# Kernel tuning notes

Measured on AMD Instinct MI355X. Metric: run time of the kernel, lower is better.

The kernel has to match this reference:

```python
import jax, jax.numpy as jnp
import numpy as np

T, B = 128, 256
E, H, C = 128, 1024, 10
VOCAB = 10


def setup_inputs() -> dict:
    key = jax.random.key(0)
    ks = jax.random.split(key, 12)
    x = jax.random.randint(ks[0], (T, B), 0, VOCAB)
    emb = jax.random.normal(ks[1], (VOCAB, E), dtype=jnp.float32)
    Wgx = jax.random.normal(ks[2], (E, H), dtype=jnp.float32) / np.sqrt(E)
    Wgh = jax.random.normal(ks[3], (H, H), dtype=jnp.float32) / np.sqrt(H)
    Wix = jax.random.normal(ks[4], (E, H), dtype=jnp.float32) / np.sqrt(E)
    Wih = jax.random.normal(ks[5], (H, H), dtype=jnp.float32) / np.sqrt(H)
    Wfx = jax.random.normal(ks[6], (E, H), dtype=jnp.float32) / np.sqrt(E)
    Wfh = jax.random.normal(ks[7], (H, H), dtype=jnp.float32) / np.sqrt(H)
    Wox = jax.random.normal(ks[8], (E, H), dtype=jnp.float32) / np.sqrt(E)
    Woh = jax.random.normal(ks[9], (H, H), dtype=jnp.float32) / np.sqrt(H)
    Wph = jax.random.normal(ks[10], (H, C), dtype=jnp.float32) / np.sqrt(H)
    bg = jnp.zeros((H,), jnp.float32)
    bi = jnp.zeros((H,), jnp.float32)
    bf = jnp.zeros((H,), jnp.float32)
    bo = jnp.zeros((H,), jnp.float32)
    bp = jnp.zeros((C,), jnp.float32)
    return dict(x=x, emb=emb, Wgx=Wgx, Wgh=Wgh, Wix=Wix, Wih=Wih, Wfx=Wfx,
                Wfh=Wfh, Wox=Wox, Woh=Woh, bg=bg, bi=bi, bf=bf, bo=bo,
                Wph=Wph, bp=bp)


def reference(x, emb, Wgx, Wgh, Wix, Wih, Wfx, Wfh, Wox, Woh,
              bg, bi, bf, bo, Wph, bp):
    Bsz = x.shape[1]
    Hn = Wgh.shape[0]
    # Fuse the 8 gate matmuls into 2 GEMMs per step (same math, concat order g,i,f,o)
    Wx = jnp.concatenate([Wgx, Wix, Wfx, Wox], axis=1)  # [E, 4H]
    Wh = jnp.concatenate([Wgh, Wih, Wfh, Woh], axis=1)  # [H, 4H]
    b = jnp.concatenate([bg, bi, bf, bo], axis=0)        # [4H]

    def step(carry, xt):
        state, hidden = carry
        e = emb[xt]                                      # [B, E]
        pre = e @ Wx + hidden @ Wh + b                   # [B, 4H]
        g = jnp.tanh(pre[:, :Hn])
        i = jax.nn.sigmoid(pre[:, Hn:2 * Hn])
        f = jax.nn.sigmoid(pre[:, 2 * Hn:3 * Hn])
        o = jax.nn.sigmoid(pre[:, 3 * Hn:])
        state = g * i + state * f
        hidden = jnp.tanh(state) * o
        return (state, hidden), None

    init = (jnp.zeros((Bsz, Hn), jnp.float32), jnp.zeros((Bsz, Hn), jnp.float32))
    (state, hidden), _ = jax.lax.scan(step, init, x)
    # Original detaches hidden/state before the output projection
    hidden = jax.lax.stop_gradient(hidden)
    return hidden @ Wph + bp                             # [B, C]
```

## Files before the change

kernel.cpp:

```cpp
#include <hip/hip_runtime.h>

typedef __bf16 bf16;
typedef __bf16 bf16x8 __attribute__((ext_vector_type(8)));
typedef float  f32x4  __attribute__((ext_vector_type(4)));

#define T_STEPS 128
#define BATCH   256
#define HD      1024
#define N4H     4096
#define EMB_D   128

__device__ __forceinline__ float fast_sigmoid(float x) {
    return 1.0f / (1.0f + __expf(-x));
}
__device__ __forceinline__ float fast_tanh(float x) {
    return 1.0f - 2.0f / (__expf(2.0f * x) + 1.0f);
}

__global__ void build_P(const float* __restrict__ emb,
                        const float* __restrict__ Wgx, const float* __restrict__ Wix,
                        const float* __restrict__ Wfx, const float* __restrict__ Wox,
                        const float* __restrict__ bg,  const float* __restrict__ bi,
                        const float* __restrict__ bfv, const float* __restrict__ bo,
                        float* __restrict__ P)
{
    int n = blockIdx.x * 256 + threadIdx.x;
    int v  = n >> 12;
    int nn = n & (N4H - 1);
    int hcol = nn >> 2, gate = nn & 3;
    const float* Wx = (gate == 0) ? Wgx : (gate == 1) ? Wix : (gate == 2) ? Wfx : Wox;
    const float* bb = (gate == 0) ? bg  : (gate == 1) ? bi  : (gate == 2) ? bfv : bo;
    float s = bb[hcol];
    for (int e = 0; e < EMB_D; ++e)
        s += emb[v * EMB_D + e] * Wx[e * HD + hcol];
    P[n] = s;
}

__global__ void build_W(const float* __restrict__ Wgh, const float* __restrict__ Wih,
                        const float* __restrict__ Wfh, const float* __restrict__ Woh,
                        bf16* __restrict__ WhpT)
{
    __shared__ float tile[64][65];
    int bid  = blockIdx.x;
    int gate = bid >> 8;
    int t2   = bid & 255;
    int kt = t2 >> 4, ht = t2 & 15;
    const float* W = (gate == 0) ? Wgh : (gate == 1) ? Wih : (gate == 2) ? Wfh : Woh;
    int tid = threadIdx.x;
    #pragma unroll
    for (int it = 0; it < 16; ++it) {
        int idx = it * 256 + tid;
        int kk = idx >> 6, hh = idx & 63;
        tile[kk][hh] = W[(size_t)(kt * 64 + kk) * HD + ht * 64 + hh];
    }
    __syncthreads();
    #pragma unroll
    for (int it = 0; it < 16; ++it) {
        int idx = it * 256 + tid;
        int hh = idx >> 6, kk = idx & 63;
        int n = (ht * 64 + hh) * 4 + gate;
        WhpT[(size_t)n * HD + kt * 64 + kk] = (bf16)tile[kk][hh];
    }
}

__global__ __launch_bounds__(512, 2)
void lstm_main(const int* __restrict__ x, const float* __restrict__ P,
               const bf16* __restrict__ WhpT, bf16* __restrict__ hbuf,
               int* __restrict__ ctl)
{
    __shared__ bf16  Blds[32][1024];
    __shared__ float red[4][64][20];

    const int tid  = threadIdx.x;
    const int lane = tid & 63;
    const int wid  = tid >> 6;
    const int w    = wid & 3;
    const int kh   = wid >> 2;
    const int frow = lane & 15;
    const int kgrp = lane >> 4;
    const int bid  = blockIdx.x;
    const int g    = bid >> 5;
    const int j    = bid & 31;

    int* bar = ctl + g * 16;

    const bf16* Abase = WhpT + (size_t)(j * 128 + w * 32 + frow) * HD + kh * 512 + kgrp * 8;
    bf16x8 Ar[2][16];
    #pragma unroll
    for (int fn = 0; fn < 2; ++fn)
        #pragma unroll
        for (int ks = 0; ks < 16; ++ks)
            Ar[fn][ks] = *(const bf16x8*)(Abase + fn * 16 * HD + ks * 32);

    const int pn0  = j * 128 + w * 32 + kgrp * 4;
    const int hc0  = j * 32 + w * 8 + kgrp;
    const int mr0  = g * 32 + frow;
    const int xorf = frow & 7;
    char* BB = (char*)&Blds[0][0];

    float st[2][2] = {{0.f, 0.f}, {0.f, 0.f}};

    for (int t = 0; t < T_STEPS; ++t) {
        f32x4 acc[2][2];
        if (kh == 0) {
            int xv0 = x[t * BATCH + mr0];
            int xv1 = x[t * BATCH + mr0 + 16];
            acc[0][0] = *(const f32x4*)(P + (size_t)xv0 * N4H + pn0);
            acc[0][1] = *(const f32x4*)(P + (size_t)xv1 * N4H + pn0);
            acc[1][0] = *(const f32x4*)(P + (size_t)xv0 * N4H + pn0 + 16);
            acc[1][1] = *(const f32x4*)(P + (size_t)xv1 * N4H + pn0 + 16);
        } else {
            f32x4 z = {0.f, 0.f, 0.f, 0.f};
            acc[0][0] = z; acc[0][1] = z; acc[1][0] = z; acc[1][1] = z;
        }

        if (t > 0) {
            if (tid == 0) {
                const int tgt = 32 * t;
                long guard = 0;
                while (__hip_atomic_load(bar, __ATOMIC_RELAXED, __HIP_MEMORY_SCOPE_AGENT) < tgt
                       && ++guard < (1L << 24)) {}
            }
            __syncthreads();
            const char* src = (const char*)(hbuf + (size_t)(t & 1) * BATCH * HD
                                                 + (size_t)g * 32 * HD);
            f32x4 stg[8];
            #pragma unroll
            for (int i2 = 0; i2 < 8; ++i2)
                asm volatile("global_load_dwordx4 %0, %1, off sc0 sc1"
                             : "=v"(stg[i2]) : "v"(src + (i2 * 512 + tid) * 16));
            asm volatile("s_waitcnt vmcnt(0)" ::: "memory");
            #pragma unroll
            for (int i2 = 0; i2 < 8; ++i2) {
                int c = i2 * 512 + tid;
                int row = c >> 7, cg = c & 127;
                *(f32x4*)(BB + row * 2048 + ((cg ^ (row & 7)) << 4)) = stg[i2];
            }
            __syncthreads();
            #pragma unroll
            for (int ks = 0; ks < 16; ++ks) {
                int off = ((kh * 64 + ks * 4 + kgrp) ^ xorf) << 4;
                bf16x8 b0 = *(const bf16x8*)(BB + frow * 2048 + off);
                bf16x8 b1 = *(const bf16x8*)(BB + (frow + 16) * 2048 + off);
                acc[0][0] = __builtin_amdgcn_mfma_f32_16x16x32_bf16(Ar[0][ks], b0, acc[0][0], 0, 0, 0);
                acc[0][1] = __builtin_amdgcn_mfma_f32_16x16x32_bf16(Ar[0][ks], b1, acc[0][1], 0, 0, 0);
                acc[1][0] = __builtin_amdgcn_mfma_f32_16x16x32_bf16(Ar[1][ks], b0, acc[1][0], 0, 0, 0);
                acc[1][1] = __builtin_amdgcn_mfma_f32_16x16x32_bf16(Ar[1][ks], b1, acc[1][1], 0, 0, 0);
            }
        }

        if (kh == 1) {
            float* rb = &red[w][lane][0];
            *(f32x4*)(rb + 0)  = acc[0][0];
            *(f32x4*)(rb + 4)  = acc[0][1];
            *(f32x4*)(rb + 8)  = acc[1][0];
            *(f32x4*)(rb + 12) = acc[1][1];
        }
        __syncthreads();
        if (kh == 0) {
            const float* rb = &red[w][lane][0];
            acc[0][0] += *(const f32x4*)(rb + 0);
            acc[0][1] += *(const f32x4*)(rb + 4);
            acc[1][0] += *(const f32x4*)(rb + 8);
            acc[1][1] += *(const f32x4*)(rb + 12);
            bf16* hout = hbuf + (size_t)((t + 1) & 1) * BATCH * HD;
            #pragma unroll
            for (int fn = 0; fn < 2; ++fn)
                #pragma unroll
                for (int fm = 0; fm < 2; ++fm) {
                    f32x4 pre = acc[fn][fm];
                    float gg = fast_tanh(pre[0]);
                    float ii = fast_sigmoid(pre[1]);
                    float ff = fast_sigmoid(pre[2]);
                    float oo = fast_sigmoid(pre[3]);
                    float s = gg * ii + st[fn][fm] * ff;
                    st[fn][fm] = s;
                    bf16 hv = (bf16)(fast_tanh(s) * oo);
                    unsigned hv32 = (unsigned)__builtin_bit_cast(unsigned short, hv);
                    const bf16* hp = hout + (size_t)(mr0 + fm * 16) * HD + hc0 + fn * 4;
                    asm volatile("global_store_short %0, %1, off sc0 sc1"
                                 :: "v"(hp), "v"(hv32) : "memory");
                }
        }
        __syncthreads();
        if (tid == 0 && t < T_STEPS - 1)
            __hip_atomic_fetch_add(bar, 1, __ATOMIC_RELAXED, __HIP_MEMORY_SCOPE_AGENT);
    }
}

__global__ void proj_out(const bf16* __restrict__ h, const float* __restrict__ Wph,
                         const float* __restrict__ bp, float* __restrict__ out)
{
    __shared__ float red[256][10];
    int b = blockIdx.x, tid = threadIdx.x;
    float acc[10];
    #pragma unroll
    for (int c = 0; c < 10; ++c) acc[c] = 0.f;
    for (int k = tid; k < HD; k += 256) {
        float hv = (float)h[(size_t)b * HD + k];
        #pragma unroll
        for (int c = 0; c < 10; ++c)
            acc[c] += hv * Wph[k * 10 + c];
    }
    #pragma unroll
    for (int c = 0; c < 10; ++c) red[tid][c] = acc[c];
    __syncthreads();
    for (int s = 128; s > 0; s >>= 1) {
        if (tid < s) {
            #pragma unroll
            for (int c = 0; c < 10; ++c) red[tid][c] += red[tid + s][c];
        }
        __syncthreads();
    }
    if (tid < 10) out[b * 10 + tid] = red[0][tid] + bp[tid];
}

extern "C" void kernel_launch(void* const* d_in, const int* in_sizes, int n_in,
                              void* d_out, int out_size, void* d_ws, size_t ws_size,
                              hipStream_t stream)
{
    const int*   x   = (const int*)  d_in[0];
    const float* emb = (const float*)d_in[1];
    const float* Wgx = (const float*)d_in[2];
    const float* Wgh = (const float*)d_in[3];
    const float* Wix = (const float*)d_in[4];
    const float* Wih = (const float*)d_in[5];
    const float* Wfx = (const float*)d_in[6];
    const float* Wfh = (const float*)d_in[7];
    const float* Wox = (const float*)d_in[8];
    const float* Woh = (const float*)d_in[9];
    const float* bg  = (const float*)d_in[10];
    const float* bi  = (const float*)d_in[11];
    const float* bfv = (const float*)d_in[12];
    const float* bo  = (const float*)d_in[13];
    const float* Wph = (const float*)d_in[14];
    const float* bp  = (const float*)d_in[15];

    char* ws = (char*)d_ws;
    bf16*  WhpT = (bf16*)ws;
    float* P    = (float*)(ws + 8388608);
    bf16*  hbuf = (bf16*)(ws + 8388608 + 163840);
    int*   ctl  = (int*)(ws + 8388608 + 163840 + 1048576);

    hipMemsetAsync(ctl, 0, 8 * 16 * sizeof(int), stream);
    build_P<<<160, 256, 0, stream>>>(emb, Wgx, Wix, Wfx, Wox, bg, bi, bfv, bo, P);
    build_W<<<1024, 256, 0, stream>>>(Wgh, Wih, Wfh, Woh, WhpT);

    void* args[] = { (void*)&x, (void*)&P, (void*)&WhpT, (void*)&hbuf, (void*)&ctl };
    hipLaunchCooperativeKernel((void*)lstm_main, dim3(256), dim3(512), args, 0, stream);

    proj_out<<<256, 256, 0, stream>>>(hbuf, Wph, bp, (float*)d_out);
}
```

Measured before the change: 610.8 us.

## Split gate epilogue across both K-halves and prefetch next-step input projection

Each warp now owns one 16-row half of its output tile and exchanges the partial sums for the other half through shared memory. Both K-halves therefore do the cross-half reduction and half of the gate nonlinearities, instead of half the warps idling through the epilogue. The next step's embedding-projection values are loaded after the h store so their latency overlaps the barrier wait. The padded reduction buffer with stride 9 and scalar stores may add LDS instructions, and the empty asm pins on the register weights could affect register allocation.

```diff
diff --git a/kernel.cpp b/kernel.cpp
--- a/kernel.cpp
+++ b/kernel.cpp
@@ -69,7 +69,7 @@
                int* __restrict__ ctl)
 {
     __shared__ bf16  Blds[32][1024];
-    __shared__ float red[4][64][20];
+    __shared__ float red[8][64][9];
 
     const int tid  = threadIdx.x;
     const int lane = tid & 63;
@@ -84,35 +84,42 @@
 
     int* bar = ctl + g * 16;
 
-    const bf16* Abase = WhpT + (size_t)(j * 128 + w * 32 + frow) * HD + kh * 512 + kgrp * 8;
-    bf16x8 Ar[2][16];
-    #pragma unroll
-    for (int fn = 0; fn < 2; ++fn)
-        #pragma unroll
-        for (int ks = 0; ks < 16; ++ks)
-            Ar[fn][ks] = *(const bf16x8*)(Abase + fn * 16 * HD + ks * 32);
-
-    const int pn0  = j * 128 + w * 32 + kgrp * 4;
-    const int hc0  = j * 32 + w * 8 + kgrp;
-    const int mr0  = g * 32 + frow;
+    const int rowO = j * 128 + w * 32 + kh * 16 + frow;
+    const int rowX = j * 128 + w * 32 + (1 - kh) * 16 + frow;
+    const bf16* AbO = WhpT + (size_t)rowO * HD + kh * 512 + kgrp * 8;
+    const bf16* AbX = WhpT + (size_t)rowX * HD + kh * 512 + kgrp * 8;
+    bf16x8 ArO[16], ArX[16];
+    #pragma unroll
+    for (int ks = 0; ks < 16; ++ks) {
+        ArO[ks] = *(const bf16x8*)(AbO + ks * 32);
+        ArX[ks] = *(const bf16x8*)(AbX + ks * 32);
+    }
+    #pragma unroll
+    for (int ks = 0; ks < 16; ++ks) {
+        asm volatile("" : "+v"(ArO[ks]));
+        asm volatile("" : "+v"(ArX[ks]));
+    }
+
+    const int mr0 = g * 32 + frow;
+    const int pnb = j * 128 + w * 32 + kh * 16 + kgrp * 4;
+    const int hcb = j * 32 + w * 8 + kh * 4 + kgrp;
     const int xorf = frow & 7;
     char* BB = (char*)&Blds[0][0];
-
-    float st[2][2] = {{0.f, 0.f}, {0.f, 0.f}};
+    float* rw = &red[0][0][0] + ((size_t)(wid ^ 4) * 64 + lane) * 9;
+    const float* rr = &red[0][0][0] + ((size_t)wid * 64 + lane) * 9;
+
+    float st0 = 0.f, st1 = 0.f;
+    f32x4 accP0, accP1;
+    {
+        int xv0 = x[mr0], xv1 = x[mr0 + 16];
+        accP0 = *(const f32x4*)(P + (size_t)xv0 * N4H + pnb);
+        accP1 = *(const f32x4*)(P + (size_t)xv1 * N4H + pnb);
+    }
 
     for (int t = 0; t < T_STEPS; ++t) {
-        f32x4 acc[2][2];
-        if (kh == 0) {
-            int xv0 = x[t * BATCH + mr0];
-            int xv1 = x[t * BATCH + mr0 + 16];
-            acc[0][0] = *(const f32x4*)(P + (size_t)xv0 * N4H + pn0);
-            acc[0][1] = *(const f32x4*)(P + (size_t)xv1 * N4H + pn0);
-            acc[1][0] = *(const f32x4*)(P + (size_t)xv0 * N4H + pn0 + 16);
-            acc[1][1] = *(const f32x4*)(P + (size_t)xv1 * N4H + pn0 + 16);
-        } else {
-            f32x4 z = {0.f, 0.f, 0.f, 0.f};
-            acc[0][0] = z; acc[0][1] = z; acc[1][0] = z; acc[1][1] = z;
-        }
+        f32x4 accO0 = accP0, accO1 = accP1;
+        f32x4 z = {0.f, 0.f, 0.f, 0.f};
+        f32x4 accX0 = z, accX1 = z;
 
         if (t > 0) {
             if (tid == 0) {
@@ -142,46 +149,53 @@
                 int off = ((kh * 64 + ks * 4 + kgrp) ^ xorf) << 4;
                 bf16x8 b0 = *(const bf16x8*)(BB + frow * 2048 + off);
                 bf16x8 b1 = *(const bf16x8*)(BB + (frow + 16) * 2048 + off);
-                acc[0][0] = __builtin_amdgcn_mfma_f32_16x16x32_bf16(Ar[0][ks], b0, acc[0][0], 0, 0, 0);
-                acc[0][1] = __builtin_amdgcn_mfma_f32_16x16x32_bf16(Ar[0][ks], b1, acc[0][1], 0, 0, 0);
-                acc[1][0] = __builtin_amdgcn_mfma_f32_16x16x32_bf16(Ar[1][ks], b0, acc[1][0], 0, 0, 0);
-                acc[1][1] = __builtin_amdgcn_mfma_f32_16x16x32_bf16(Ar[1][ks], b1, acc[1][1], 0, 0, 0);
+                accO0 = __builtin_amdgcn_mfma_f32_16x16x32_bf16(ArO[ks], b0, accO0, 0, 0, 0);
+                accO1 = __builtin_amdgcn_mfma_f32_16x16x32_bf16(ArO[ks], b1, accO1, 0, 0, 0);
+                accX0 = __builtin_amdgcn_mfma_f32_16x16x32_bf16(ArX[ks], b0, accX0, 0, 0, 0);
+                accX1 = __builtin_amdgcn_mfma_f32_16x16x32_bf16(ArX[ks], b1, accX1, 0, 0, 0);
             }
         }
 
-        if (kh == 1) {
-            float* rb = &red[w][lane][0];
-            *(f32x4*)(rb + 0)  = acc[0][0];
-            *(f32x4*)(rb + 4)  = acc[0][1];
-            *(f32x4*)(rb + 8)  = acc[1][0];
-            *(f32x4*)(rb + 12) = acc[1][1];
-        }
+        rw[0] = accX0[0]; rw[1] = accX0[1]; rw[2] = accX0[2]; rw[3] = accX0[3];
+        rw[4] = accX1[0]; rw[5] = accX1[1]; rw[6] = accX1[2]; rw[7] = accX1[3];
         __syncthreads();
-        if (kh == 0) {
-            const float* rb = &red[w][lane][0];
-            acc[0][0] += *(const f32x4*)(rb + 0);
-            acc[0][1] += *(const f32x4*)(rb + 4);
-            acc[1][0] += *(const f32x4*)(rb + 8);
-            acc[1][1] += *(const f32x4*)(rb + 12);
-            bf16* hout = hbuf + (size_t)((t + 1) & 1) * BATCH * HD;
-            #pragma unroll
-            for (int fn = 0; fn < 2; ++fn)
-                #pragma unroll
-                for (int fm = 0; fm < 2; ++fm) {
-                    f32x4 pre = acc[fn][fm];
-                    float gg = fast_tanh(pre[0]);
-                    float ii = fast_sigmoid(pre[1]);
-                    float ff = fast_sigmoid(pre[2]);
-                    float oo = fast_sigmoid(pre[3]);
-                    float s = gg * ii + st[fn][fm] * ff;
-                    st[fn][fm] = s;
-                    bf16 hv = (bf16)(fast_tanh(s) * oo);
-                    unsigned hv32 = (unsigned)__builtin_bit_cast(unsigned short, hv);
-                    const bf16* hp = hout + (size_t)(mr0 + fm * 16) * HD + hc0 + fn * 4;
-                    asm volatile("global_store_short %0, %1, off sc0 sc1"
-                                 :: "v"(hp), "v"(hv32) : "memory");
-                }
-        }
+        accO0[0] += rr[0]; accO0[1] += rr[1]; accO0[2] += rr[2]; accO0[3] += rr[3];
+        accO1[0] += rr[4]; accO1[1] += rr[5]; accO1[2] += rr[6]; accO1[3] += rr[7];
+
+        bf16* hout = hbuf + (size_t)((t + 1) & 1) * BATCH * HD;
+        {
+            float gg = fast_tanh(accO0[0]);
+            float ii = fast_sigmoid(accO0[1]);
+            float ff = fast_sigmoid(accO0[2]);
+            float oo = fast_sigmoid(accO0[3]);
+            float s = gg * ii + st0 * ff;
+            st0 = s;
+            bf16 hv = (bf16)(fast_tanh(s) * oo);
+            unsigned hv32 = (unsigned)__builtin_bit_cast(unsigned short, hv);
+            const bf16* hp = hout + (size_t)mr0 * HD + hcb;
+            asm volatile("global_store_short %0, %1, off sc0 sc1"
+                         :: "v"(hp), "v"(hv32) : "memory");
+        }
+        {
+            float gg = fast_tanh(accO1[0]);
+            float ii = fast_sigmoid(accO1[1]);
+            float ff = fast_sigmoid(accO1[2]);
+            float oo = fast_sigmoid(accO1[3]);
+            float s = gg * ii + st1 * ff;
+            st1 = s;
+            bf16 hv = (bf16)(fast_tanh(s) * oo);
+            unsigned hv32 = (unsigned)__builtin_bit_cast(unsigned short, hv);
+            const bf16* hp = hout + (size_t)(mr0 + 16) * HD + hcb;
+            asm volatile("global_store_short %0, %1, off sc0 sc1"
+                         :: "v"(hp), "v"(hv32) : "memory");
+        }
+
+        if (t < T_STEPS - 1) {
+            int xv0 = x[(t + 1) * BATCH + mr0], xv1 = x[(t + 1) * BATCH + mr0 + 16];
+            accP0 = *(const f32x4*)(P + (size_t)xv0 * N4H + pnb);
+            accP1 = *(const f32x4*)(P + (size_t)xv1 * N4H + pnb);
+        }
+
         __syncthreads();
         if (tid == 0 && t < T_STEPS - 1)
             __hip_atomic_fetch_add(bar, 1, __ATOMIC_RELAXED, __HIP_MEMORY_SCOPE_AGENT);
```

Result: slower. 836.9 us (+37.0%).
